# Performance work log

Hardware: AMD Instinct MI355X
Metric: run time of the kernel (lower is better)

Reference implementation:

```python
import jax, jax.numpy as jnp
import numpy as np

B, S, H = 2, 2048, 2304
NH, HD, NKV = 8, 256, 4
WINDOW = 512
CAP = 50.0
THETA = 10000.0
NEG_INF = -2.3819763e38


def setup_inputs() -> dict:
    key = jax.random.key(0)
    ks = jax.random.split(key, 6)
    hidden_states = jax.random.normal(ks[0], (B, S, H), dtype=jnp.float32)
    # causal additive mask (0 where attend, -inf-ish where masked)
    i = jnp.arange(S)
    causal = i[None, :] <= i[:, None]
    attention_mask = jnp.broadcast_to(
        jnp.where(causal, 0.0, NEG_INF).astype(jnp.float32)[None, None], (B, 1, S, S)
    )
    position_ids = jnp.broadcast_to(jnp.arange(S, dtype=jnp.int32)[None], (B, S))
    scale = 0.02
    Wq = jax.random.normal(ks[1], (H, NH * HD), dtype=jnp.float32) * scale
    Wk = jax.random.normal(ks[2], (H, NKV * HD), dtype=jnp.float32) * scale
    Wv = jax.random.normal(ks[3], (H, NKV * HD), dtype=jnp.float32) * scale
    Wo = jax.random.normal(ks[4], (NH * HD, H), dtype=jnp.float32) * scale
    return {
        "hidden_states": hidden_states,
        "attention_mask": attention_mask,
        "position_ids": position_ids,
        "Wq": Wq,
        "Wk": Wk,
        "Wv": Wv,
        "Wo": Wo,
    }


def _rotate_half(x):
    h = x.shape[-1] // 2
    return jnp.concatenate([-x[..., h:], x[..., :h]], axis=-1)


def reference(hidden_states, attention_mask, position_ids, Wq, Wk, Wv, Wo):
    b, s, _ = hidden_states.shape
    q = (hidden_states @ Wq).reshape(b, s, NH, HD).transpose(0, 2, 1, 3)   # [B,NH,S,HD]
    k = (hidden_states @ Wk).reshape(b, s, NKV, HD).transpose(0, 2, 1, 3)  # [B,NKV,S,HD]
    v = (hidden_states @ Wv).reshape(b, s, NKV, HD).transpose(0, 2, 1, 3)
    # rotary embedding
    inv_freq = 1.0 / (THETA ** (jnp.arange(0, HD, 2, dtype=jnp.float32) / HD))
    freqs = position_ids.astype(jnp.float32)[..., None] * inv_freq  # [B,S,HD/2]
    emb = jnp.concatenate([freqs, freqs], axis=-1)                  # [B,S,HD]
    cos = jnp.cos(emb)[:, None]  # unsqueeze head dim
    sin = jnp.sin(emb)[:, None]
    q = q * cos + _rotate_half(q) * sin
    k = k * cos + _rotate_half(k) * sin
    # GQA: repeat kv heads
    rep = NH // NKV
    k = jnp.repeat(k, rep, axis=1)
    v = jnp.repeat(v, rep, axis=1)
    logits = jnp.einsum("bhqd,bhkd->bhqk", q, k) / jnp.sqrt(jnp.float32(HD))
    # sliding-window mask: keep |i-j| <= WINDOW-1, else NEG_INF
    idx = jnp.arange(s)
    sliding = jnp.abs(idx[:, None] - idx[None, :]) <= (WINDOW - 1)
    mask = jnp.where(sliding[None, None], attention_mask, NEG_INF)
    # tanh logit softcapping, then additive mask
    logits = jnp.tanh(logits / CAP) * CAP + mask
    probs = jax.nn.softmax(logits.astype(jnp.float32), axis=-1).astype(q.dtype)
    out = jnp.einsum("bhqk,bhkd->bhqd", probs, v)
    out = out.transpose(0, 2, 1, 3).reshape(b, s, NH * HD)
    return out @ Wo
```

## Files before the change

kernel.cpp:

```cpp
#include <hip/hip_runtime.h>
#include <cmath>

#define B_   2
#define S_   2048
#define H_   2304
#define NH_  8
#define HD_  256
#define NKV_ 4
#define WIN_ 512
#define QKVW 4096

typedef unsigned short ushort_t;
typedef __attribute__((ext_vector_type(8))) short bf16x8;
typedef __attribute__((ext_vector_type(4))) float floatx4;

__device__ __forceinline__ unsigned short f2bf(float f) {
  unsigned u = __builtin_bit_cast(unsigned, f);
  u += 0x7fff + ((u >> 16) & 1);
  return (unsigned short)(u >> 16);
}
__device__ __forceinline__ float bf2f(ushort_t v) {
  unsigned u = (unsigned)v << 16;
  return __builtin_bit_cast(float, u);
}

__device__ __forceinline__ void gl2lds16(const void* g, void* l) {
  __builtin_amdgcn_global_load_lds(
      (const __attribute__((address_space(1))) unsigned int*)g,
      (__attribute__((address_space(3))) unsigned int*)l, 16, 0, 0);
}

__global__ void cast_bf16(const float* __restrict__ in, ushort_t* __restrict__ out) {
  const int i = blockIdx.x * 256 + threadIdx.x;
  float4 v = ((const float4*)in)[i];
  ushort4 o;
  o.x = f2bf(v.x); o.y = f2bf(v.y); o.z = f2bf(v.z); o.w = f2bf(v.w);
  ((ushort4*)out)[i] = o;
}

__global__ void transpose_cast(const float* __restrict__ W, ushort_t* __restrict__ Wt,
                               int K, int N) {
  __shared__ float t[32][33];
  const int lx = threadIdx.x & 31, ly = threadIdx.x >> 5;
  const int n0 = blockIdx.x * 32, k0 = blockIdx.y * 32;
#pragma unroll
  for (int i = 0; i < 4; ++i)
    t[ly + i * 8][lx] = W[(long long)(k0 + ly + i * 8) * N + n0 + lx];
  __syncthreads();
#pragma unroll
  for (int i = 0; i < 4; ++i)
    Wt[(long long)(n0 + ly + i * 8) * K + k0 + lx] = f2bf(t[lx][ly + i * 8]);
}

#define LOAD_A(qm_) do { \
  _Pragma("unroll") for (int i_ = 0; i_ < 4; ++i_) { \
    const int row_ = wm + (qm_) * 64 + i_ * 16 + l15; \
    _Pragma("unroll") for (int kk_ = 0; kk_ < 2; ++kk_) \
      a[i_][kk_] = *(const bf16x8*)&ldsA[row_ * 64 + (((kk_ * 4 + lq) ^ (l15 & 7)) * 8)]; \
  } \
} while (0)

#define LOAD_B(qn_) do { \
  _Pragma("unroll") for (int j_ = 0; j_ < 2; ++j_) { \
    const int row_ = wn + (qn_) * 32 + j_ * 16 + l15; \
    _Pragma("unroll") for (int kk_ = 0; kk_ < 2; ++kk_) \
      b[qn_][j_][kk_] = *(const bf16x8*)&ldsB[row_ * 64 + (((kk_ * 4 + lq) ^ (l15 & 7)) * 8)]; \
  } \
} while (0)

#define MFMA_QUAD(qm_, qn_) do { \
  _Pragma("unroll") for (int kk_ = 0; kk_ < 2; ++kk_) \
  _Pragma("unroll") for (int i_ = 0; i_ < 4; ++i_) \
  _Pragma("unroll") for (int j_ = 0; j_ < 2; ++j_) \
    acc[(qm_) * 4 + i_][(qn_) * 2 + j_] = __builtin_amdgcn_mfma_f32_16x16x32_bf16( \
        a[i_][kk_], b[qn_][j_][kk_], acc[(qm_) * 4 + i_][(qn_) * 2 + j_], 0, 0, 0); \
} while (0)

#define STAGE_A(dst_, gsrc_, t_, qm_) do { \
  _Pragma("unroll") for (int jj_ = 0; jj_ < 2; ++jj_) { \
    const int g_ = w * 2 + jj_; \
    const int tr0_ = ((g_ >> 3) * 128) + (qm_) * 64 + (g_ & 7) * 8; \
    gl2lds16(gsrc_ + (size_t)tr0_ * K + (size_t)(t_) * 64 + laneOff, dst_ + tr0_ * 64); \
  } \
} while (0)

#define STAGE_B(dst_, gsrc_, t_, qn_) do { \
  _Pragma("unroll") for (int jj_ = 0; jj_ < 2; ++jj_) { \
    const int g_ = w * 2 + jj_; \
    const int tr0_ = ((g_ >> 2) * 64) + (qn_) * 32 + (g_ & 3) * 8; \
    gl2lds16(gsrc_ + (size_t)tr0_ * K + (size_t)(t_) * 64 + laneOff, dst_ + tr0_ * 64); \
  } \
} while (0)

template <bool OUT_BF16>
__launch_bounds__(512)
__global__ void gemm_8ph(const ushort_t* __restrict__ A,
                         const ushort_t* __restrict__ Bt,
                         void* __restrict__ Cv, int M, int N, int K) {
  extern __shared__ __attribute__((aligned(128))) ushort_t smem[];
  const int tid = threadIdx.x, lane = tid & 63, w = tid >> 6;
  const int wm = (w >> 2) * 128, wn = (w & 3) * 64;
  const int l15 = lane & 15, lq = lane >> 4;
  const int bm = blockIdx.y * 256, bn = blockIdx.x * 256;
  const int NT = K >> 6;

  const ushort_t* Ab = A + (size_t)bm * K;
  const ushort_t* Bb = Bt + (size_t)bn * K;
  const size_t laneOff = (size_t)(lane >> 3) * K + (size_t)(((lane & 7) ^ (lane >> 3)) * 8);

  ushort_t* A0s = smem;
  ushort_t* B0s = smem + 16384;
  ushort_t* A1s = smem + 32768;
  ushort_t* B1s = smem + 49152;

  floatx4 acc[8][4] = {};

  STAGE_A(A0s, Ab, 0, 0);
  STAGE_B(B0s, Bb, 0, 0);
  STAGE_B(B0s, Bb, 0, 1);
  STAGE_A(A0s, Ab, 0, 1);
  asm volatile("s_waitcnt vmcnt(4)" ::: "memory");
  if (NT > 1) {
    STAGE_A(A1s, Ab, 1, 0);
    STAGE_B(B1s, Bb, 1, 0);
    STAGE_B(B1s, Bb, 1, 1);
    asm volatile("s_waitcnt vmcnt(6)" ::: "memory");
  } else {
    asm volatile("s_waitcnt vmcnt(0)" ::: "memory");
  }
  __builtin_amdgcn_s_barrier();

  for (int t = 0; t < NT; ++t) {
    ushort_t* ldsA  = (t & 1) ? A1s : A0s;
    ushort_t* ldsB  = (t & 1) ? B1s : B0s;
    ushort_t* ldsAo = (t & 1) ? A0s : A1s;

    bf16x8 a[4][2], b[2][2][2];

    LOAD_A(0);
    LOAD_B(0);
    if (t + 1 < NT) STAGE_A(ldsAo, Ab, t + 1, 1);
    __builtin_amdgcn_s_barrier();
    asm volatile("s_waitcnt lgkmcnt(0)" ::: "memory");
    __builtin_amdgcn_s_setprio(1);
    MFMA_QUAD(0, 0);
    __builtin_amdgcn_s_setprio(0);
    __builtin_amdgcn_s_barrier();

    LOAD_B(1);
    if (t + 2 < NT) STAGE_A(ldsA, Ab, t + 2, 0);
    __builtin_amdgcn_s_barrier();
    asm volatile("s_waitcnt lgkmcnt(0)" ::: "memory");
    __builtin_amdgcn_s_setprio(1);
    MFMA_QUAD(0, 1);
    __builtin_amdgcn_s_setprio(0);
    __builtin_amdgcn_s_barrier();

    LOAD_A(1);
    if (t + 2 < NT) STAGE_B(ldsB, Bb, t + 2, 0);
    __builtin_amdgcn_s_barrier();
    asm volatile("s_waitcnt lgkmcnt(0)" ::: "memory");
    __builtin_amdgcn_s_setprio(1);
    MFMA_QUAD(1, 0);
    __builtin_amdgcn_s_setprio(0);
    __builtin_amdgcn_s_barrier();

    if (t + 2 < NT) STAGE_B(ldsB, Bb, t + 2, 1);
    __builtin_amdgcn_s_barrier();
    __builtin_amdgcn_s_setprio(1);
    MFMA_QUAD(1, 1);
    __builtin_amdgcn_s_setprio(0);
    if (t < NT - 1) {
      if (t == NT - 2) asm volatile("s_waitcnt vmcnt(0)" ::: "memory");
      else             asm volatile("s_waitcnt vmcnt(6)" ::: "memory");
    }
    __builtin_amdgcn_s_barrier();
  }

  const int r0 = lq * 4;
#pragma unroll
  for (int mf = 0; mf < 8; ++mf)
#pragma unroll
    for (int nf = 0; nf < 4; ++nf) {
      const long long base = (long long)(bm + wm + mf * 16 + r0) * N + bn + wn + nf * 16 + l15;
      if (OUT_BF16) {
        ushort_t* Cp = (ushort_t*)Cv + base;
#pragma unroll
        for (int rr = 0; rr < 4; ++rr) Cp[(long long)rr * N] = f2bf(acc[mf][nf][rr]);
      } else {
        float* Cp = (float*)Cv + base;
#pragma unroll
        for (int rr = 0; rr < 4; ++rr) Cp[(long long)rr * N] = acc[mf][nf][rr];
      }
    }
}

#undef LOAD_A
#undef LOAD_B
#undef MFMA_QUAD
#undef STAGE_A
#undef STAGE_B

template <bool OUT_BF16>
__launch_bounds__(256)
__global__ void gemm_bt(const ushort_t* __restrict__ A,
                        const ushort_t* __restrict__ Bt,
                        void* __restrict__ Cv, int M, int N, int K) {
  __shared__ ushort_t As[128 * 64];
  __shared__ ushort_t Bs[128 * 64];
  const int tid = threadIdx.x, lane = tid & 63, wid = tid >> 6;
  const int bm = blockIdx.y * 128, bn = blockIdx.x * 128;
  const int wm = (wid >> 1) * 64, wn = (wid & 1) * 64;

  floatx4 acc[4][4] = {};

  const int r  = tid >> 1;
  const int cp = (tid & 1) * 4;
  const int wkey = r & 7;
  const ushort_t* Ap = A  + (long long)(bm + r) * K + cp * 8;
  const ushort_t* Bp = Bt + (long long)(bn + r) * K + cp * 8;
  ushort_t* Aw = &As[r * 64];
  ushort_t* Bw = &Bs[r * 64];

  const int l15 = lane & 15, lq = lane >> 4;
  const int rkey = l15 & 7;

  bf16x8 ar[4], br[4];
#pragma unroll
  for (int i = 0; i < 4; ++i) {
    ar[i] = *(const bf16x8*)(Ap + i * 8);
    br[i] = *(const bf16x8*)(Bp + i * 8);
  }

  for (int k0 = 0; k0 < K; k0 += 64) {
    __syncthreads();
#pragma unroll
    for (int i = 0; i < 4; ++i) {
      *(bf16x8*)&Aw[((cp + i) ^ wkey) * 8] = ar[i];
      *(bf16x8*)&Bw[((cp + i) ^ wkey) * 8] = br[i];
    }
    __syncthreads();

    if (k0 + 64 < K) {
      const int kn = k0 + 64;
#pragma unroll
      for (int i = 0; i < 4; ++i) {
        ar[i] = *(const bf16x8*)(Ap + kn + i * 8);
        br[i] = *(const bf16x8*)(Bp + kn + i * 8);
      }
    }

#pragma unroll
    for (int kk = 0; kk < 2; ++kk) {
      bf16x8 af[4], bfr[4];
#pragma unroll
      for (int i = 0; i < 4; ++i) {
        af[i]  = *(const bf16x8*)&As[(wm + i * 16 + l15) * 64 + ((kk * 4 + lq) ^ rkey) * 8];
        bfr[i] = *(const bf16x8*)&Bs[(wn + i * 16 + l15) * 64 + ((kk * 4 + lq) ^ rkey) * 8];
      }
#pragma unroll
      for (int i = 0; i < 4; ++i)
#pragma unroll
        for (int j = 0; j < 4; ++j)
          acc[i][j] = __builtin_amdgcn_mfma_f32_16x16x32_bf16(af[i], bfr[j], acc[i][j], 0, 0, 0);
    }
  }

  const int r0 = lq * 4, c0 = l15;
#pragma unroll
  for (int i = 0; i < 4; ++i)
#pragma unroll
    for (int j = 0; j < 4; ++j) {
      const long long base = (long long)(bm + wm + i * 16 + r0) * N + bn + wn + j * 16 + c0;
      if (OUT_BF16) {
        ushort_t* Cp = (ushort_t*)Cv + base;
#pragma unroll
        for (int rr = 0; rr < 4; ++rr) Cp[(long long)rr * N] = f2bf(acc[i][j][rr]);
      } else {
        float* Cp = (float*)Cv + base;
#pragma unroll
        for (int rr = 0; rr < 4; ++rr) Cp[(long long)rr * N] = acc[i][j][rr];
      }
    }
}

__global__ void rope_inplace(ushort_t* __restrict__ QKV16, const int* __restrict__ pos) {
  const int bs  = blockIdx.x;
  const int gid = blockIdx.y * 256 + threadIdx.x;
  const int head = gid >> 7;
  const int d    = gid & 127;
  const float pp   = (float)pos[bs];
  const float invf = __expf(-(float)d * (9.210340371976184f / 128.0f));
  const float ang  = pp * invf;
  const float cc = cosf(ang), sn = sinf(ang);
  ushort_t* base = QKV16 + (size_t)bs * QKVW + head * HD_;
  const float x1 = bf2f(base[d]);
  const float x2 = bf2f(base[d + 128]);
  float o1 = x1 * cc - x2 * sn;
  float o2 = x2 * cc + x1 * sn;
  if (head < NH_) { o1 *= 0.0625f; o2 *= 0.0625f; }
  base[d]       = f2bf(o1);
  base[d + 128] = f2bf(o2);
}

__global__ void v_prep(const ushort_t* __restrict__ QKV16, ushort_t* __restrict__ Vt16) {
  __shared__ ushort_t tile[32][33];
  const int k0 = blockIdx.x * 32, d0 = blockIdx.y * 32;
  const int b = blockIdx.z >> 2, hk = blockIdx.z & 3;
  const int lx = threadIdx.x & 31, ly = threadIdx.x >> 5;
#pragma unroll
  for (int i = 0; i < 4; ++i)
    tile[ly + 8 * i][lx] =
        QKV16[(size_t)(b * S_ + k0 + ly + 8 * i) * QKVW + 3072 + hk * HD_ + d0 + lx];
  __syncthreads();
#pragma unroll
  for (int i = 0; i < 4; ++i)
    Vt16[((size_t)(b * NKV_ + hk) * HD_ + d0 + ly + 8 * i) * S_ + k0 + lx] =
        tile[lx][ly + 8 * i];
}

__launch_bounds__(512)
__global__ void attn_mfma(const ushort_t* __restrict__ QKV16,
                          const ushort_t* __restrict__ Vt16,
                          ushort_t* __restrict__ AOb) {
  __shared__ ushort_t Ks[32 * 256];
  __shared__ ushort_t Vts[256 * 32];
  __shared__ ushort_t Ps[8][16 * 32];
  __shared__ float rsb[8][16];

  const int lane = threadIdx.x & 63, w = threadIdx.x >> 6;
  const int l15 = lane & 15, lq = lane >> 4;
  const int qb = blockIdx.x * 64;
  const int hp = blockIdx.y, b = blockIdx.z;
  const int h  = hp * 2 + (w >> 2);
  const int hw = w & 3;

  const ushort_t* Qh = QKV16 + (size_t)b * S_ * QKVW + h * HD_;
  const ushort_t* Kh = QKV16 + (size_t)b * S_ * QKVW + 2048 + hp * HD_;
  const ushort_t* Vh = Vt16 + ((size_t)(b * NKV_ + hp) * HD_) * S_;

  const int qw = qb + hw * 16;

  bf16x8 afq[8];
  {
    const ushort_t* qr = Qh + (size_t)(qw + l15) * QKVW + lq * 8;
#pragma unroll
    for (int kd = 0; kd < 8; ++kd) afq[kd] = *(const bf16x8*)(qr + kd * 32);
  }

  floatx4 acc[16] = {};
  float rs[4] = {0.f, 0.f, 0.f, 0.f};

  int kb0 = qb - (WIN_ - 1);
  if (kb0 < 0) kb0 = 0;
  kb0 &= ~31;

  const int ksp = lane & 31, ksr = lane >> 5;
  const int vsp = lane & 3,  vsr = lane >> 2;

  for (int kb = kb0; kb < qb + 64; kb += 32) {
    __syncthreads();
#pragma unroll
    for (int i = 0; i < 2; ++i) {
      const int kl = w * 4 + 2 * i + ksr;
      gl2lds16(Kh + (size_t)(kb + kl) * QKVW + (ksp ^ (kl & 31)) * 8,
               &Ks[(w * 4 + 2 * i) * 256]);
    }
#pragma unroll
    for (int i = 0; i < 2; ++i) {
      const int dl = w * 32 + 16 * i + vsr;
      gl2lds16(Vh + (size_t)dl * S_ + kb + (vsp ^ ((dl >> 1) & 3)) * 8,
               &Vts[(w * 32 + 16 * i) * 32]);
    }
    __syncthreads();

    if (kb <= qw + 15 && kb + 31 >= qw - (WIN_ - 1)) {
      ushort_t* Pw = Ps[w];
#pragma unroll
      for (int kt = 0; kt < 2; ++kt) {
        floatx4 sacc = {};
        const int keyl = kt * 16 + l15;
        const int krow = keyl * 256;
        const int ksw = keyl & 31;
#pragma unroll
        for (int kd = 0; kd < 8; ++kd) {
          bf16x8 bk = *(const bf16x8*)&Ks[krow + ((kd * 4 + lq) ^ ksw) * 8];
          sacc = __builtin_amdgcn_mfma_f32_16x16x32_bf16(afq[kd], bk, sacc, 0, 0, 0);
        }
        const int keyg = kb + keyl;
#pragma unroll
        for (int rr = 0; rr < 4; ++rr) {
          const int qg = qw + lq * 4 + rr;
          const float t = __expf(sacc[rr] * 0.04f);
          const float L = 50.f - __fdividef(100.f, t + 1.f);
          float p = __expf(L);
          p = (keyg <= qg && keyg >= qg - (WIN_ - 1)) ? p : 0.f;
          rs[rr] += p;
          const int ql = lq * 4 + rr;
          const int ch = kt * 2 + (l15 >> 3);
          Pw[ql * 32 + ((ch ^ ((ql >> 1) & 3)) * 8) + (l15 & 7)] = f2bf(p);
        }
      }
      asm volatile("s_waitcnt lgkmcnt(0)" ::: "memory");

      const bf16x8 bp = *(const bf16x8*)&Pw[l15 * 32 + ((lq ^ ((l15 >> 1) & 3)) * 8)];
      const int vsw = (l15 >> 1) & 3;
#pragma unroll
      for (int t = 0; t < 16; ++t) {
        bf16x8 av = *(const bf16x8*)&Vts[(t * 16 + l15) * 32 + ((lq ^ vsw) * 8)];
        acc[t] = __builtin_amdgcn_mfma_f32_16x16x32_bf16(av, bp, acc[t], 0, 0, 0);
      }
    }
  }

#pragma unroll
  for (int rr = 0; rr < 4; ++rr) {
    rs[rr] += __shfl_xor(rs[rr], 1, 64);
    rs[rr] += __shfl_xor(rs[rr], 2, 64);
    rs[rr] += __shfl_xor(rs[rr], 4, 64);
    rs[rr] += __shfl_xor(rs[rr], 8, 64);
  }
  if (l15 == 0) {
#pragma unroll
    for (int rr = 0; rr < 4; ++rr) rsb[w][lq * 4 + rr] = rs[rr];
  }
  asm volatile("s_waitcnt lgkmcnt(0)" ::: "memory");
  __builtin_amdgcn_wave_barrier();
  const float inv = 1.0f / rsb[w][l15];

  const size_t ob = ((size_t)(b * S_ + qw + l15) * NH_ + h) * HD_;
#pragma unroll
  for (int t = 0; t < 16; ++t) {
    ushort4 o;
    o.x = f2bf(acc[t][0] * inv);
    o.y = f2bf(acc[t][1] * inv);
    o.z = f2bf(acc[t][2] * inv);
    o.w = f2bf(acc[t][3] * inv);
    *(ushort4*)&AOb[ob + t * 16 + lq * 4] = o;
  }
}

extern "C" void kernel_launch(void* const* d_in, const int* in_sizes, int n_in,
                              void* d_out, int out_size, void* d_ws, size_t ws_size,
                              hipStream_t stream) {
  const float* X   = (const float*)d_in[0];
  const int*   pos = (const int*)d_in[2];
  const float* Wq  = (const float*)d_in[3];
  const float* Wk  = (const float*)d_in[4];
  const float* Wv  = (const float*)d_in[5];
  const float* Wo  = (const float*)d_in[6];
  float* out = (float*)d_out;

  const int M  = B_ * S_;
  const int NQ = NH_ * HD_;
  const int NK = NKV_ * HD_;

  char* w = (char*)d_ws;
  ushort_t* QKV16 = (ushort_t*)w;  w += (size_t)M * QKVW * 2;
  ushort_t* Xb    = (ushort_t*)w;  w += (size_t)M * H_ * 2;
  ushort_t* Wqkvt = (ushort_t*)w;  w += (size_t)QKVW * H_ * 2;
  ushort_t* Wot   = (ushort_t*)w;  w += (size_t)H_ * NQ * 2;
  ushort_t* Vt16  = (ushort_t*)w;  w += (size_t)B_ * NKV_ * S_ * HD_ * 2;
  ushort_t* AOb   = (ushort_t*)w;  w += (size_t)M * NQ * 2;

  static bool g_init = false, g_8ph_ok = false;
  if (!g_init) {
    hipError_t e1 = hipFuncSetAttribute(
        reinterpret_cast<const void*>(&gemm_8ph<true>),
        hipFuncAttributeMaxDynamicSharedMemorySize, 131072);
    hipError_t e2 = hipFuncSetAttribute(
        reinterpret_cast<const void*>(&gemm_8ph<false>),
        hipFuncAttributeMaxDynamicSharedMemorySize, 131072);
    g_8ph_ok = (e1 == hipSuccess && e2 == hipSuccess);
    g_init = true;
  }

  dim3 blk(256);

  cast_bf16<<<(M * H_) / 1024, blk, 0, stream>>>(X, Xb);
  transpose_cast<<<dim3(NQ / 32, H_ / 32), blk, 0, stream>>>(Wq, Wqkvt, H_, NQ);
  transpose_cast<<<dim3(NK / 32, H_ / 32), blk, 0, stream>>>(Wk, Wqkvt + (size_t)2048 * H_, H_, NK);
  transpose_cast<<<dim3(NK / 32, H_ / 32), blk, 0, stream>>>(Wv, Wqkvt + (size_t)3072 * H_, H_, NK);
  transpose_cast<<<dim3(H_ / 32, NQ / 32), blk, 0, stream>>>(Wo, Wot, NQ, H_);

  if (g_8ph_ok) {
    gemm_8ph<true><<<dim3(QKVW / 256, M / 256), dim3(512), 131072, stream>>>(
        Xb, Wqkvt, QKV16, M, QKVW, H_);
  } else {
    gemm_bt<true><<<dim3(QKVW / 128, M / 128), blk, 0, stream>>>(Xb, Wqkvt, QKV16, M, QKVW, H_);
  }

  rope_inplace<<<dim3(M, 6), blk, 0, stream>>>(QKV16, pos);
  v_prep<<<dim3(S_ / 32, HD_ / 32, B_ * NKV_), blk, 0, stream>>>(QKV16, Vt16);

  attn_mfma<<<dim3(S_ / 64, NKV_, B_), dim3(512), 0, stream>>>(QKV16, Vt16, AOb);

  if (g_8ph_ok) {
    gemm_8ph<false><<<dim3(H_ / 256, M / 256), dim3(512), 131072, stream>>>(
        AOb, Wot, out, M, H_, NQ);
  } else {
    gemm_bt<false><<<dim3(H_ / 128, M / 128), blk, 0, stream>>>(AOb, Wot, out, M, H_, NQ);
  }
}
```

Baseline: 363.4 us.

## Prefetch LDS fragments across phases and swizzle workgroup order in GEMM

Restructures the 8-phase GEMM main loop so the LDS reads for the next quadrant (and for the next K-tile) are issued right after each MFMA batch, keeping two B register sets and reordering the quadrant sequence to (0,0),(0,1),(1,1),(1,0). This hides LDS read latency behind MFMA work and drops some barriers. It also remaps workgroup IDs with an XCD-aware swizzle so neighbouring tiles land on the same chiplet for better L2 reuse. In exchange it raises register pressure and makes the vmcnt waits more intricate, so a wrong count could cause races.

```diff
diff --git a/kernel.cpp b/kernel.cpp
--- a/kernel.cpp
+++ b/kernel.cpp
@@ -52,28 +52,28 @@
     Wt[(long long)(n0 + ly + i * 8) * K + k0 + lx] = f2bf(t[lx][ly + i * 8]);
 }
 
-#define LOAD_A(qm_) do { \
+#define LDA_FROM(base_, qm_) do { \
   _Pragma("unroll") for (int i_ = 0; i_ < 4; ++i_) { \
     const int row_ = wm + (qm_) * 64 + i_ * 16 + l15; \
     _Pragma("unroll") for (int kk_ = 0; kk_ < 2; ++kk_) \
-      a[i_][kk_] = *(const bf16x8*)&ldsA[row_ * 64 + (((kk_ * 4 + lq) ^ (l15 & 7)) * 8)]; \
+      aR[i_][kk_] = *(const bf16x8*)&(base_)[row_ * 64 + (((kk_ * 4 + lq) ^ (l15 & 7)) * 8)]; \
   } \
 } while (0)
 
-#define LOAD_B(qn_) do { \
+#define LDB_FROM(base_, dst_, qn_) do { \
   _Pragma("unroll") for (int j_ = 0; j_ < 2; ++j_) { \
     const int row_ = wn + (qn_) * 32 + j_ * 16 + l15; \
     _Pragma("unroll") for (int kk_ = 0; kk_ < 2; ++kk_) \
-      b[qn_][j_][kk_] = *(const bf16x8*)&ldsB[row_ * 64 + (((kk_ * 4 + lq) ^ (l15 & 7)) * 8)]; \
+      dst_[j_][kk_] = *(const bf16x8*)&(base_)[row_ * 64 + (((kk_ * 4 + lq) ^ (l15 & 7)) * 8)]; \
   } \
 } while (0)
 
-#define MFMA_QUAD(qm_, qn_) do { \
+#define MFMA_QUAD(qm_, qn_, breg_) do { \
   _Pragma("unroll") for (int kk_ = 0; kk_ < 2; ++kk_) \
   _Pragma("unroll") for (int i_ = 0; i_ < 4; ++i_) \
   _Pragma("unroll") for (int j_ = 0; j_ < 2; ++j_) \
     acc[(qm_) * 4 + i_][(qn_) * 2 + j_] = __builtin_amdgcn_mfma_f32_16x16x32_bf16( \
-        a[i_][kk_], b[qn_][j_][kk_], acc[(qm_) * 4 + i_][(qn_) * 2 + j_], 0, 0, 0); \
+        aR[i_][kk_], breg_[j_][kk_], acc[(qm_) * 4 + i_][(qn_) * 2 + j_], 0, 0, 0); \
 } while (0)
 
 #define STAGE_A(dst_, gsrc_, t_, qm_) do { \
@@ -91,6 +91,9 @@
     gl2lds16(gsrc_ + (size_t)tr0_ * K + (size_t)(t_) * 64 + laneOff, dst_ + tr0_ * 64); \
   } \
 } while (0)
+
+#define SB0() __builtin_amdgcn_sched_barrier(0)
+#define LGKM0() do { asm volatile("s_waitcnt lgkmcnt(0)" ::: "memory"); SB0(); } while (0)
 
 template <bool OUT_BF16>
 __launch_bounds__(512)
@@ -101,7 +104,13 @@
   const int tid = threadIdx.x, lane = tid & 63, w = tid >> 6;
   const int wm = (w >> 2) * 128, wn = (w & 3) * 64;
   const int l15 = lane & 15, lq = lane >> 4;
-  const int bm = blockIdx.y * 256, bn = blockIdx.x * 256;
+
+  const int nwg  = gridDim.x * gridDim.y;
+  const int orig = blockIdx.y * gridDim.x + blockIdx.x;
+  const int cpx  = nwg >> 3;
+  const int swz  = (orig & 7) * cpx + (orig >> 3);
+  const int bx   = swz % gridDim.x, by = swz / gridDim.x;
+  const int bm = by * 256, bn = bx * 256;
   const int NT = K >> 6;
 
   const ushort_t* Ab = A + (size_t)bm * K;
@@ -114,12 +123,12 @@
   ushort_t* B1s = smem + 49152;
 
   floatx4 acc[8][4] = {};
+  bf16x8 aR[4][2], b0[2][2], b1[2][2];
 
   STAGE_A(A0s, Ab, 0, 0);
   STAGE_B(B0s, Bb, 0, 0);
   STAGE_B(B0s, Bb, 0, 1);
   STAGE_A(A0s, Ab, 0, 1);
-  asm volatile("s_waitcnt vmcnt(4)" ::: "memory");
   if (NT > 1) {
     STAGE_A(A1s, Ab, 1, 0);
     STAGE_B(B1s, Bb, 1, 0);
@@ -129,50 +138,53 @@
     asm volatile("s_waitcnt vmcnt(0)" ::: "memory");
   }
   __builtin_amdgcn_s_barrier();
+  LDA_FROM(A0s, 0);
+  LDB_FROM(B0s, b0, 0);
 
   for (int t = 0; t < NT; ++t) {
     ushort_t* ldsA  = (t & 1) ? A1s : A0s;
     ushort_t* ldsB  = (t & 1) ? B1s : B0s;
     ushort_t* ldsAo = (t & 1) ? A0s : A1s;
-
-    bf16x8 a[4][2], b[2][2][2];
-
-    LOAD_A(0);
-    LOAD_B(0);
+    ushort_t* ldsBo = (t & 1) ? B0s : B1s;
+
+    LGKM0();
     if (t + 1 < NT) STAGE_A(ldsAo, Ab, t + 1, 1);
+    __builtin_amdgcn_s_setprio(1);
+    MFMA_QUAD(0, 0, b0);
+    __builtin_amdgcn_s_setprio(0);
+    SB0();
+    LDB_FROM(ldsB, b1, 1);
     __builtin_amdgcn_s_barrier();
-    asm volatile("s_waitcnt lgkmcnt(0)" ::: "memory");
+
+    LGKM0();
+    if (t + 2 < NT) STAGE_A(ldsA, Ab, t + 2, 0);
     __builtin_amdgcn_s_setprio(1);
-    MFMA_QUAD(0, 0);
+    MFMA_QUAD(0, 1, b1);
     __builtin_amdgcn_s_setprio(0);
+    SB0();
+    LDA_FROM(ldsA, 1);
     __builtin_amdgcn_s_barrier();
 
-    LOAD_B(1);
-    if (t + 2 < NT) STAGE_A(ldsA, Ab, t + 2, 0);
+    LGKM0();
+    if (t + 2 < NT) STAGE_B(ldsB, Bb, t + 2, 0);
+    __builtin_amdgcn_s_setprio(1);
+    MFMA_QUAD(1, 1, b1);
+    __builtin_amdgcn_s_setprio(0);
+    SB0();
+    if (t + 1 < NT) {
+      if (t == NT - 2) asm volatile("s_waitcnt vmcnt(0)" ::: "memory");
+      else             asm volatile("s_waitcnt vmcnt(4)" ::: "memory");
+    }
     __builtin_amdgcn_s_barrier();
-    asm volatile("s_waitcnt lgkmcnt(0)" ::: "memory");
+
+    if (t + 2 < NT) STAGE_B(ldsB, Bb, t + 2, 1);
     __builtin_amdgcn_s_setprio(1);
-    MFMA_QUAD(0, 1);
+    MFMA_QUAD(1, 0, b0);
     __builtin_amdgcn_s_setprio(0);
-    __builtin_amdgcn_s_barrier();
-
-    LOAD_A(1);
-    if (t + 2 < NT) STAGE_B(ldsB, Bb, t + 2, 0);
-    __builtin_amdgcn_s_barrier();
-    asm volatile("s_waitcnt lgkmcnt(0)" ::: "memory");
-    __builtin_amdgcn_s_setprio(1);
-    MFMA_QUAD(1, 0);
-    __builtin_amdgcn_s_setprio(0);
-    __builtin_amdgcn_s_barrier();
-
-    if (t + 2 < NT) STAGE_B(ldsB, Bb, t + 2, 1);
-    __builtin_amdgcn_s_barrier();
-    __builtin_amdgcn_s_setprio(1);
-    MFMA_QUAD(1, 1);
-    __builtin_amdgcn_s_setprio(0);
-    if (t < NT - 1) {
-      if (t == NT - 2) asm volatile("s_waitcnt vmcnt(0)" ::: "memory");
-      else             asm volatile("s_waitcnt vmcnt(6)" ::: "memory");
+    SB0();
+    if (t + 1 < NT) {
+      LDA_FROM(ldsAo, 0);
+      LDB_FROM(ldsBo, b0, 0);
     }
     __builtin_amdgcn_s_barrier();
   }
@@ -195,8 +207,8 @@
     }
 }
 
-#undef LOAD_A
-#undef LOAD_B
+#undef LDA_FROM
+#undef LDB_FROM
 #undef MFMA_QUAD
 #undef STAGE_A
 #undef STAGE_B
```

After: 357.3 us. About the same (-1.7%).
